# Optimization experiments

Hardware: AMD Instinct MI355X
Metric: run time of the kernel (lower is better)

## Reference

```python
import jax, jax.numpy as jnp
import numpy as np

B, S, H = 4, 2048, 768
NUM_POS = B * (S // 4)  # fixed count of positive clc_label entries (2048, even)
NEG_BIG = -1000000000.0


def setup_inputs() -> dict:
    key = jax.random.key(0)
    k1, k2, k3, k4, k5 = jax.random.split(key, 5)
    encoded_states = jax.random.normal(k1, (B, S, H), dtype=jnp.float32)
    # sorted cell-ids -> contiguous segments for the equality mask
    indicator = jnp.sort(jax.random.randint(k2, (B, S), 0, 256, dtype=jnp.int32), axis=-1)
    # clc_label: first S//4 positions per row are positive targets (class ids in [1,S)),
    # last S//2 positions are -1 (attendable keys), rest 0 (ignored)
    pos_labels = jax.random.randint(k3, (B, S // 4), 1, S, dtype=jnp.int32)
    clc_label = jnp.zeros((B, S), dtype=jnp.int32)
    clc_label = clc_label.at[:, : S // 4].set(pos_labels)
    clc_label = clc_label.at[:, S // 2:].set(-1)
    # uniform_linear params (torch Linear: y = x @ W.T + b)
    W = jax.random.normal(k4, (H, H), dtype=jnp.float32) / np.sqrt(H)
    b = jax.random.normal(k5, (H,), dtype=jnp.float32) * 0.01
    return {"encoded_states": encoded_states, "W": W, "b": b,
            "indicator": indicator, "clc_label": clc_label}


def _ce(logits, labels):
    # mean cross entropy; all labels are > 0 here so ignore_index=0 never triggers
    logp = jax.nn.log_softmax(logits, axis=-1)
    return -jnp.take_along_axis(logp, labels[:, None], axis=1).mean()


def reference(encoded_states, W, b, indicator, clc_label):
    # indicator-equality mask matmul == within-segment sum (the segment-reduce emulation)
    seg_mask = (indicator[:, :, None] == indicator[:, None, :]).astype(encoded_states.dtype)  # [B,S,S]
    agg = jnp.einsum("bij,bjh->bih", seg_mask, encoded_states)  # [B,S,H]
    # Q and K use the SAME linear on the same input -> compute once
    proj = jnp.tanh(agg @ W.T + b)  # [B,S,H]
    scores = jnp.einsum("bih,bjh->bij", proj, proj)  # [B,S,S]
    # attend only to positions where clc_label < 0
    allow = (clc_label < 0)[:, None, :]  # [B,1,S]
    scores = scores + jnp.where(allow, 0.0, NEG_BIG).astype(scores.dtype)
    flat = scores.reshape(-1, S)          # [B*S, S]
    labels = clc_label.reshape(-1)        # [B*S]
    pos_idx = jnp.nonzero(labels > 0, size=NUM_POS)[0]  # row-major order == torch bool-indexing
    logits = flat[pos_idx]                # [NUM_POS, S]
    labs = labels[pos_idx]                # [NUM_POS]
    sep_logits, sep_labels = logits[0::2], labs[0::2]
    tok_logits, tok_labels = logits[1::2], labs[1::2]
    sep_loss = _ce(sep_logits, sep_labels)
    tok_loss = _ce(tok_logits, tok_labels)
    sep_correct = jnp.sum((jnp.argmax(sep_logits, axis=-1).astype(jnp.int32) == sep_labels).astype(jnp.float32))
    tok_correct = jnp.sum((jnp.argmax(tok_logits, axis=-1).astype(jnp.int32) == tok_labels).astype(jnp.float32))
    sep_count = jnp.asarray(sep_logits.shape[0] + 1e-6, dtype=jnp.float32)
    tok_count = jnp.asarray(tok_logits.shape[0] + 1e-6, dtype=jnp.float32)
    return ((sep_loss, sep_correct, sep_count), (tok_loss, tok_correct, tok_count))
```

## Files before the change

### kernel.cpp

```cpp
#include <hip/hip_runtime.h>
#include <math.h>
#include <limits.h>

#define BB 4
#define SS 2048
#define HH 768
#define MAXSEG 256
#define NUM_POS (BB*(SS/4))
#define NEG_BIG -1000000000.0f

typedef _Float16 f16x8 __attribute__((ext_vector_type(8)));
typedef _Float16 f16x4 __attribute__((ext_vector_type(4)));
typedef float    f32x4 __attribute__((ext_vector_type(4)));

__global__ __launch_bounds__(256) void k_scan(
    const int* __restrict__ ind, const int* __restrict__ clc,
    int* __restrict__ seg_id, int* __restrict__ seg_start,
    int* __restrict__ nseg, int* __restrict__ pos_local, int* __restrict__ pos_cnt,
    int* __restrict__ allowCnt, int* __restrict__ firstAllow)
{
  int b = blockIdx.x, t = threadIdx.x;
  int lane = t & 63, wid = t >> 6;
  __shared__ int sInd[SS];
  __shared__ int sWave[4];
  __shared__ int sAC[MAXSEG];
  __shared__ int sFA[MAXSEG];
  for (int i = t; i < SS; i += 256) sInd[i] = ind[b*SS + i];
  sAC[t] = 0; sFA[t] = INT_MAX;
  __syncthreads();

  int i0 = t * 8;
  int f[8], cv[8];
  int lsum = 0;
  #pragma unroll
  for (int u = 0; u < 8; u++) {
    int i = i0 + u;
    f[u] = (i == 0) ? 0 : (sInd[i] != sInd[i-1]);
    cv[u] = clc[b*SS + i];
    lsum += f[u];
  }
  int x = lsum;
  #pragma unroll
  for (int off = 1; off < 64; off <<= 1) {
    int v = __shfl_up(x, off, 64);
    if (lane >= off) x += v;
  }
  if (lane == 63) sWave[wid] = x;
  __syncthreads();
  int base = 0;
  for (int w = 0; w < wid; w++) base += sWave[w];
  int run = base + x - lsum;
  int rid[8];
  #pragma unroll
  for (int u = 0; u < 8; u++) {
    int i = i0 + u;
    run += f[u];
    rid[u] = run;
    seg_id[b*SS + i] = run;
    if (f[u] || i == 0) seg_start[b*(MAXSEG+1) + run] = i;
  }
  if (t == 255) { nseg[b] = run + 1; seg_start[b*(MAXSEG+1) + run + 1] = SS; }

  #pragma unroll
  for (int u = 0; u < 8; u++) {
    if (cv[u] < 0) {
      atomicAdd(&sAC[rid[u]], 1);
      atomicMin(&sFA[rid[u]], i0 + u);
    }
  }
  __syncthreads();
  allowCnt[b*MAXSEG + t]   = sAC[t];
  firstAllow[b*MAXSEG + t] = sFA[t];

  int psum = 0;
  int p[8];
  #pragma unroll
  for (int u = 0; u < 8; u++) { p[u] = (cv[u] > 0) ? 1 : 0; psum += p[u]; }
  x = psum;
  #pragma unroll
  for (int off = 1; off < 64; off <<= 1) {
    int v = __shfl_up(x, off, 64);
    if (lane >= off) x += v;
  }
  __syncthreads();
  if (lane == 63) sWave[wid] = x;
  __syncthreads();
  base = 0;
  for (int w = 0; w < wid; w++) base += sWave[w];
  int rank = base + x - psum;
  #pragma unroll
  for (int u = 0; u < 8; u++) {
    if (p[u]) { pos_local[b*SS + rank] = i0 + u; rank++; }
  }
  if (t == 255) pos_cnt[b] = rank;
}

__global__ __launch_bounds__(256) void k_segsum(
    const float* __restrict__ es, const float* __restrict__ W,
    const int* __restrict__ seg_start, const int* __restrict__ nseg,
    _Float16* __restrict__ segsum_h, _Float16* __restrict__ Wh)
{
  int blk = blockIdx.x, t = threadIdx.x;
  if (blk >= BB*MAXSEG) {
    int idx = (blk - BB*MAXSEG)*256 + t;
    float4 v = ((const float4*)W)[idx];
    f16x4 h;
    h[0] = (_Float16)v.x; h[1] = (_Float16)v.y;
    h[2] = (_Float16)v.z; h[3] = (_Float16)v.w;
    *(f16x4*)(Wh + (size_t)idx*4) = h;
    return;
  }
  int b = blk >> 8, s = blk & 255;
  _Float16* o = segsum_h + ((size_t)b*MAXSEG + s)*HH;
  if (s >= nseg[b]) {
    o[t] = (_Float16)0.f; o[t+256] = (_Float16)0.f; o[t+512] = (_Float16)0.f;
    return;
  }
  int st = seg_start[b*(MAXSEG+1) + s];
  int en = seg_start[b*(MAXSEG+1) + s + 1];
  const float* base = es + (size_t)b*SS*HH;
  float a0 = 0.f, a1 = 0.f, a2 = 0.f;
  for (int i = st; i < en; i++) {
    const float* r = base + (size_t)i*HH;
    a0 += r[t]; a1 += r[t+256]; a2 += r[t+512];
  }
  o[t] = (_Float16)a0; o[t+256] = (_Float16)a1; o[t+512] = (_Float16)a2;
}

__global__ __launch_bounds__(256) void k_gemmU(
    const _Float16* __restrict__ Ah, const _Float16* __restrict__ Wh,
    const float* __restrict__ bias, _Float16* __restrict__ Uh)
{
  int tid = threadIdx.x;
  int w = tid >> 6, lane = tid & 63;
  int tile = blockIdx.x*4 + w;
  int tm = tile / 24, tn = tile % 24;
  int rb = tm*32, cb = tn*32;
  int m0 = lane & 15, quad = lane >> 4;
  const _Float16* A0 = Ah + (size_t)(rb + m0)*HH + quad*8;
  const _Float16* A1 = A0 + (size_t)16*HH;
  const _Float16* B0 = Wh + (size_t)(cb + m0)*HH + quad*8;
  const _Float16* B1 = B0 + (size_t)16*HH;
  f32x4 acc00 = {0.f,0.f,0.f,0.f}, acc01 = {0.f,0.f,0.f,0.f};
  f32x4 acc10 = {0.f,0.f,0.f,0.f}, acc11 = {0.f,0.f,0.f,0.f};
  #pragma unroll 4
  for (int k0 = 0; k0 < HH; k0 += 32) {
    f16x8 a0 = *(const f16x8*)(A0 + k0);
    f16x8 a1 = *(const f16x8*)(A1 + k0);
    f16x8 b0 = *(const f16x8*)(B0 + k0);
    f16x8 b1 = *(const f16x8*)(B1 + k0);
    acc00 = __builtin_amdgcn_mfma_f32_16x16x32_f16(a0, b0, acc00, 0, 0, 0);
    acc01 = __builtin_amdgcn_mfma_f32_16x16x32_f16(a0, b1, acc01, 0, 0, 0);
    acc10 = __builtin_amdgcn_mfma_f32_16x16x32_f16(a1, b0, acc10, 0, 0, 0);
    acc11 = __builtin_amdgcn_mfma_f32_16x16x32_f16(a1, b1, acc11, 0, 0, 0);
  }
  float bc0 = bias[cb + m0], bc1 = bias[cb + 16 + m0];
  int r0 = rb + quad*4;
  #pragma unroll
  for (int i = 0; i < 4; i++) {
    Uh[(size_t)(r0+i)*HH    + cb + m0]      = (_Float16)tanhf(acc00[i] + bc0);
    Uh[(size_t)(r0+i)*HH    + cb + 16 + m0] = (_Float16)tanhf(acc01[i] + bc1);
    Uh[(size_t)(r0+16+i)*HH + cb + m0]      = (_Float16)tanhf(acc10[i] + bc0);
    Uh[(size_t)(r0+16+i)*HH + cb + 16 + m0] = (_Float16)tanhf(acc11[i] + bc1);
  }
}

__global__ __launch_bounds__(256) void k_gram(
    const _Float16* __restrict__ Uh, float* __restrict__ G)
{
  int tid = threadIdx.x;
  int w = tid >> 6, lane = tid & 63;
  int tile = blockIdx.x*4 + w;
  int b = tile >> 8, rem = tile & 255;
  int rb = (rem >> 4)*16, cb = (rem & 15)*16;
  int m0 = lane & 15, quad = lane >> 4;
  const _Float16* Ub = Uh + (size_t)b*MAXSEG*HH;
  const _Float16* A0 = Ub + (size_t)(rb + m0)*HH + quad*8;
  const _Float16* B0 = Ub + (size_t)(cb + m0)*HH + quad*8;
  f32x4 acc = {0.f,0.f,0.f,0.f};
  #pragma unroll 4
  for (int k0 = 0; k0 < HH; k0 += 32) {
    f16x8 a  = *(const f16x8*)(A0 + k0);
    f16x8 bb = *(const f16x8*)(B0 + k0);
    acc = __builtin_amdgcn_mfma_f32_16x16x32_f16(a, bb, acc, 0, 0, 0);
  }
  float* Gb = G + (size_t)b*MAXSEG*MAXSEG;
  int r0 = rb + quad*4;
  #pragma unroll
  for (int i = 0; i < 4; i++)
    Gb[(size_t)(r0+i)*MAXSEG + cb + m0] = acc[i];
}

__global__ __launch_bounds__(256) void k_seglse(
    const float* __restrict__ G, const int* __restrict__ allowCnt,
    const int* __restrict__ firstAllow, const int* __restrict__ nseg,
    float* __restrict__ lse, int* __restrict__ amax)
{
  int lane = threadIdx.x & 63, wid = threadIdx.x >> 6;
  int row = blockIdx.x * 4 + wid;
  int b = row >> 8, si = row & 255;
  if (si >= nseg[b]) return;
  const float* g = G + ((size_t)b*MAXSEG + si)*MAXSEG;
  const int* ac = allowCnt + b*MAXSEG;
  const int* fa = firstAllow + b*MAXSEG;

  float gv[4]; int av[4], fv[4];
  #pragma unroll
  for (int q = 0; q < 4; q++) {
    int s = lane + 64*q;
    gv[q] = g[s]; av[q] = ac[s]; fv[q] = fa[s];
  }
  float m = -INFINITY;
  #pragma unroll
  for (int q = 0; q < 4; q++) if (av[q] > 0) m = fmaxf(m, gv[q]);
  #pragma unroll
  for (int off = 32; off > 0; off >>= 1) m = fmaxf(m, __shfl_xor(m, off, 64));
  float s = 0.f;
  #pragma unroll
  for (int q = 0; q < 4; q++) if (av[q] > 0) s += (float)av[q] * expf(gv[q] - m);
  #pragma unroll
  for (int off = 32; off > 0; off >>= 1) s += __shfl_xor(s, off, 64);
  float bv = -INFINITY; int bi = INT_MAX;
  #pragma unroll
  for (int q = 0; q < 4; q++) {
    if (av[q] > 0 && (gv[q] > bv || (gv[q] == bv && fv[q] < bi))) { bv = gv[q]; bi = fv[q]; }
  }
  #pragma unroll
  for (int off = 32; off > 0; off >>= 1) {
    float ov = __shfl_xor(bv, off, 64);
    int   oi = __shfl_xor(bi, off, 64);
    if (ov > bv || (ov == bv && oi < bi)) { bv = ov; bi = oi; }
  }
  if (lane == 0) {
    lse[row]  = m + logf(s);
    amax[row] = bi;
  }
}

__global__ __launch_bounds__(256) void k_posfinal(
    const float* __restrict__ G, const int* __restrict__ seg_id,
    const int* __restrict__ clc, const int* __restrict__ pos_local,
    const int* __restrict__ pos_cnt, const float* __restrict__ lse,
    const int* __restrict__ amax, float* __restrict__ out)
{
  __shared__ int sBase[BB+1];
  __shared__ float sL0[4], sC0[4], sL1[4], sC1[4];
  int t = threadIdx.x;
  if (t == 0) {
    int acc = 0; sBase[0] = 0;
    for (int b = 0; b < BB; b++) { acc += pos_cnt[b]; sBase[b+1] = acc; }
  }
  __syncthreads();
  int total = sBase[BB];
  if (total > NUM_POS) total = NUM_POS;
  float l0 = 0.f, c0 = 0.f, l1 = 0.f, c1 = 0.f;
  for (int r = t; r < total; r += 256) {
    int b = 0;
    while (b < BB-1 && r >= sBase[b+1]) b++;
    int k = r - sBase[b];
    int i  = pos_local[b*SS + k];
    int si = seg_id[b*SS + i];
    int L  = clc[b*SS + i];
    int sL = seg_id[b*SS + L];
    float vL = G[((size_t)b*MAXSEG + si)*MAXSEG + sL] + (clc[b*SS + L] < 0 ? 0.0f : NEG_BIG);
    float loss = lse[b*MAXSEG + si] - vL;
    float corr = (amax[b*MAXSEG + si] == L) ? 1.0f : 0.0f;
    if (r & 1) { l1 += loss; c1 += corr; } else { l0 += loss; c0 += corr; }
  }
  int lane = t & 63, wid = t >> 6;
  #pragma unroll
  for (int off = 32; off > 0; off >>= 1) {
    l0 += __shfl_down(l0, off, 64);
    c0 += __shfl_down(c0, off, 64);
    l1 += __shfl_down(l1, off, 64);
    c1 += __shfl_down(c1, off, 64);
  }
  if (lane == 0) { sL0[wid] = l0; sC0[wid] = c0; sL1[wid] = l1; sC1[wid] = c1; }
  __syncthreads();
  if (t == 0) {
    float L0 = sL0[0]+sL0[1]+sL0[2]+sL0[3];
    float C0 = sC0[0]+sC0[1]+sC0[2]+sC0[3];
    float L1 = sL1[0]+sL1[1]+sL1[2]+sL1[3];
    float C1 = sC1[0]+sC1[1]+sC1[2]+sC1[3];
    float n = (float)(NUM_POS/2);
    out[0] = L0 / n;
    out[1] = C0;
    out[2] = n + 1e-6f;
    out[3] = L1 / n;
    out[4] = C1;
    out[5] = n + 1e-6f;
  }
}

extern "C" void kernel_launch(void* const* d_in, const int* in_sizes, int n_in,
                              void* d_out, int out_size, void* d_ws, size_t ws_size,
                              hipStream_t stream)
{
  const float* es   = (const float*)d_in[0];
  const float* W    = (const float*)d_in[1];
  const float* bias = (const float*)d_in[2];
  const int*   ind  = (const int*)d_in[3];
  const int*   clc  = (const int*)d_in[4];
  float* out = (float*)d_out;

  char* ws = (char*)d_ws;
  int*   nseg       = (int*)(ws + 0);
  int*   pos_cnt    = (int*)(ws + 256);
  int*   seg_start  = (int*)(ws + 1024);
  int*   seg_id     = (int*)(ws + 8192);
  int*   pos_local  = (int*)(ws + 40960);
  int*   allowCnt   = (int*)(ws + 73728);
  int*   firstAllow = (int*)(ws + 77824);
  float* lse        = (float*)(ws + 81920);
  int*   amax       = (int*)(ws + 86016);
  _Float16* segsum_h = (_Float16*)(ws + 90112);
  _Float16* Wh       = (_Float16*)(ws + 1662976);
  _Float16* Uh       = (_Float16*)(ws + 2842624);
  float*    G        = (float*)(ws + 4415488);

  k_scan<<<BB, 256, 0, stream>>>(ind, clc, seg_id, seg_start, nseg, pos_local,
                                 pos_cnt, allowCnt, firstAllow);
  k_segsum<<<BB*MAXSEG + 576, 256, 0, stream>>>(es, W, seg_start, nseg, segsum_h, Wh);
  k_gemmU<<<192, 256, 0, stream>>>(segsum_h, Wh, bias, Uh);
  k_gram<<<256, 256, 0, stream>>>(Uh, G);
  k_seglse<<<(BB*MAXSEG)/4, 256, 0, stream>>>(G, allowCnt, firstAllow, nseg, lse, amax);
  k_posfinal<<<1, 256, 0, stream>>>(G, seg_id, clc, pos_local, pos_cnt, lse, amax, out);
}
```

Before: 122.9 us.

## Fuse six kernel stages into one cooperative persistent kernel with grid syncs

```diff
diff --git a/kernel.cpp b/kernel.cpp
--- a/kernel.cpp
+++ b/kernel.cpp
@@ -1,6 +1,9 @@
 #include <hip/hip_runtime.h>
+#include <hip/hip_cooperative_groups.h>
 #include <math.h>
 #include <limits.h>
+
+namespace cg = cooperative_groups;
 
 #define BB 4
 #define SS 2048
@@ -13,297 +16,12 @@
 typedef _Float16 f16x4 __attribute__((ext_vector_type(4)));
 typedef float    f32x4 __attribute__((ext_vector_type(4)));
 
-__global__ __launch_bounds__(256) void k_scan(
-    const int* __restrict__ ind, const int* __restrict__ clc,
-    int* __restrict__ seg_id, int* __restrict__ seg_start,
-    int* __restrict__ nseg, int* __restrict__ pos_local, int* __restrict__ pos_cnt,
-    int* __restrict__ allowCnt, int* __restrict__ firstAllow)
+__global__ __launch_bounds__(256, 2) void k_fused(
+    const float* __restrict__ es, const float* __restrict__ W,
+    const float* __restrict__ bias, const int* __restrict__ ind,
+    const int* __restrict__ clc, float* __restrict__ out,
+    char* __restrict__ ws)
 {
-  int b = blockIdx.x, t = threadIdx.x;
-  int lane = t & 63, wid = t >> 6;
-  __shared__ int sInd[SS];
-  __shared__ int sWave[4];
-  __shared__ int sAC[MAXSEG];
-  __shared__ int sFA[MAXSEG];
-  for (int i = t; i < SS; i += 256) sInd[i] = ind[b*SS + i];
-  sAC[t] = 0; sFA[t] = INT_MAX;
-  __syncthreads();
-
-  int i0 = t * 8;
-  int f[8], cv[8];
-  int lsum = 0;
-  #pragma unroll
-  for (int u = 0; u < 8; u++) {
-    int i = i0 + u;
-    f[u] = (i == 0) ? 0 : (sInd[i] != sInd[i-1]);
-    cv[u] = clc[b*SS + i];
-    lsum += f[u];
-  }
-  int x = lsum;
-  #pragma unroll
-  for (int off = 1; off < 64; off <<= 1) {
-    int v = __shfl_up(x, off, 64);
-    if (lane >= off) x += v;
-  }
-  if (lane == 63) sWave[wid] = x;
-  __syncthreads();
-  int base = 0;
-  for (int w = 0; w < wid; w++) base += sWave[w];
-  int run = base + x - lsum;
-  int rid[8];
-  #pragma unroll
-  for (int u = 0; u < 8; u++) {
-    int i = i0 + u;
-    run += f[u];
-    rid[u] = run;
-    seg_id[b*SS + i] = run;
-    if (f[u] || i == 0) seg_start[b*(MAXSEG+1) + run] = i;
-  }
-  if (t == 255) { nseg[b] = run + 1; seg_start[b*(MAXSEG+1) + run + 1] = SS; }
-
-  #pragma unroll
-  for (int u = 0; u < 8; u++) {
-    if (cv[u] < 0) {
-      atomicAdd(&sAC[rid[u]], 1);
-      atomicMin(&sFA[rid[u]], i0 + u);
-    }
-  }
-  __syncthreads();
-  allowCnt[b*MAXSEG + t]   = sAC[t];
-  firstAllow[b*MAXSEG + t] = sFA[t];
-
-  int psum = 0;
-  int p[8];
-  #pragma unroll
-  for (int u = 0; u < 8; u++) { p[u] = (cv[u] > 0) ? 1 : 0; psum += p[u]; }
-  x = psum;
-  #pragma unroll
-  for (int off = 1; off < 64; off <<= 1) {
-    int v = __shfl_up(x, off, 64);
-    if (lane >= off) x += v;
-  }
-  __syncthreads();
-  if (lane == 63) sWave[wid] = x;
-  __syncthreads();
-  base = 0;
-  for (int w = 0; w < wid; w++) base += sWave[w];
-  int rank = base + x - psum;
-  #pragma unroll
-  for (int u = 0; u < 8; u++) {
-    if (p[u]) { pos_local[b*SS + rank] = i0 + u; rank++; }
-  }
-  if (t == 255) pos_cnt[b] = rank;
-}
-
-__global__ __launch_bounds__(256) void k_segsum(
-    const float* __restrict__ es, const float* __restrict__ W,
-    const int* __restrict__ seg_start, const int* __restrict__ nseg,
-    _Float16* __restrict__ segsum_h, _Float16* __restrict__ Wh)
-{
-  int blk = blockIdx.x, t = threadIdx.x;
-  if (blk >= BB*MAXSEG) {
-    int idx = (blk - BB*MAXSEG)*256 + t;
-    float4 v = ((const float4*)W)[idx];
-    f16x4 h;
-    h[0] = (_Float16)v.x; h[1] = (_Float16)v.y;
-    h[2] = (_Float16)v.z; h[3] = (_Float16)v.w;
-    *(f16x4*)(Wh + (size_t)idx*4) = h;
-    return;
-  }
-  int b = blk >> 8, s = blk & 255;
-  _Float16* o = segsum_h + ((size_t)b*MAXSEG + s)*HH;
-  if (s >= nseg[b]) {
-    o[t] = (_Float16)0.f; o[t+256] = (_Float16)0.f; o[t+512] = (_Float16)0.f;
-    return;
-  }
-  int st = seg_start[b*(MAXSEG+1) + s];
-  int en = seg_start[b*(MAXSEG+1) + s + 1];
-  const float* base = es + (size_t)b*SS*HH;
-  float a0 = 0.f, a1 = 0.f, a2 = 0.f;
-  for (int i = st; i < en; i++) {
-    const float* r = base + (size_t)i*HH;
-    a0 += r[t]; a1 += r[t+256]; a2 += r[t+512];
-  }
-  o[t] = (_Float16)a0; o[t+256] = (_Float16)a1; o[t+512] = (_Float16)a2;
-}
-
-__global__ __launch_bounds__(256) void k_gemmU(
-    const _Float16* __restrict__ Ah, const _Float16* __restrict__ Wh,
-    const float* __restrict__ bias, _Float16* __restrict__ Uh)
-{
-  int tid = threadIdx.x;
-  int w = tid >> 6, lane = tid & 63;
-  int tile = blockIdx.x*4 + w;
-  int tm = tile / 24, tn = tile % 24;
-  int rb = tm*32, cb = tn*32;
-  int m0 = lane & 15, quad = lane >> 4;
-  const _Float16* A0 = Ah + (size_t)(rb + m0)*HH + quad*8;
-  const _Float16* A1 = A0 + (size_t)16*HH;
-  const _Float16* B0 = Wh + (size_t)(cb + m0)*HH + quad*8;
-  const _Float16* B1 = B0 + (size_t)16*HH;
-  f32x4 acc00 = {0.f,0.f,0.f,0.f}, acc01 = {0.f,0.f,0.f,0.f};
-  f32x4 acc10 = {0.f,0.f,0.f,0.f}, acc11 = {0.f,0.f,0.f,0.f};
-  #pragma unroll 4
-  for (int k0 = 0; k0 < HH; k0 += 32) {
-    f16x8 a0 = *(const f16x8*)(A0 + k0);
-    f16x8 a1 = *(const f16x8*)(A1 + k0);
-    f16x8 b0 = *(const f16x8*)(B0 + k0);
-    f16x8 b1 = *(const f16x8*)(B1 + k0);
-    acc00 = __builtin_amdgcn_mfma_f32_16x16x32_f16(a0, b0, acc00, 0, 0, 0);
-    acc01 = __builtin_amdgcn_mfma_f32_16x16x32_f16(a0, b1, acc01, 0, 0, 0);
-    acc10 = __builtin_amdgcn_mfma_f32_16x16x32_f16(a1, b0, acc10, 0, 0, 0);
-    acc11 = __builtin_amdgcn_mfma_f32_16x16x32_f16(a1, b1, acc11, 0, 0, 0);
-  }
-  float bc0 = bias[cb + m0], bc1 = bias[cb + 16 + m0];
-  int r0 = rb + quad*4;
-  #pragma unroll
-  for (int i = 0; i < 4; i++) {
-    Uh[(size_t)(r0+i)*HH    + cb + m0]      = (_Float16)tanhf(acc00[i] + bc0);
-    Uh[(size_t)(r0+i)*HH    + cb + 16 + m0] = (_Float16)tanhf(acc01[i] + bc1);
-    Uh[(size_t)(r0+16+i)*HH + cb + m0]      = (_Float16)tanhf(acc10[i] + bc0);
-    Uh[(size_t)(r0+16+i)*HH + cb + 16 + m0] = (_Float16)tanhf(acc11[i] + bc1);
-  }
-}
-
-__global__ __launch_bounds__(256) void k_gram(
-    const _Float16* __restrict__ Uh, float* __restrict__ G)
-{
-  int tid = threadIdx.x;
-  int w = tid >> 6, lane = tid & 63;
-  int tile = blockIdx.x*4 + w;
-  int b = tile >> 8, rem = tile & 255;
-  int rb = (rem >> 4)*16, cb = (rem & 15)*16;
-  int m0 = lane & 15, quad = lane >> 4;
-  const _Float16* Ub = Uh + (size_t)b*MAXSEG*HH;
-  const _Float16* A0 = Ub + (size_t)(rb + m0)*HH + quad*8;
-  const _Float16* B0 = Ub + (size_t)(cb + m0)*HH + quad*8;
-  f32x4 acc = {0.f,0.f,0.f,0.f};
-  #pragma unroll 4
-  for (int k0 = 0; k0 < HH; k0 += 32) {
-    f16x8 a  = *(const f16x8*)(A0 + k0);
-    f16x8 bb = *(const f16x8*)(B0 + k0);
-    acc = __builtin_amdgcn_mfma_f32_16x16x32_f16(a, bb, acc, 0, 0, 0);
-  }
-  float* Gb = G + (size_t)b*MAXSEG*MAXSEG;
-  int r0 = rb + quad*4;
-  #pragma unroll
-  for (int i = 0; i < 4; i++)
-    Gb[(size_t)(r0+i)*MAXSEG + cb + m0] = acc[i];
-}
-
-__global__ __launch_bounds__(256) void k_seglse(
-    const float* __restrict__ G, const int* __restrict__ allowCnt,
-    const int* __restrict__ firstAllow, const int* __restrict__ nseg,
-    float* __restrict__ lse, int* __restrict__ amax)
-{
-  int lane = threadIdx.x & 63, wid = threadIdx.x >> 6;
-  int row = blockIdx.x * 4 + wid;
-  int b = row >> 8, si = row & 255;
-  if (si >= nseg[b]) return;
-  const float* g = G + ((size_t)b*MAXSEG + si)*MAXSEG;
-  const int* ac = allowCnt + b*MAXSEG;
-  const int* fa = firstAllow + b*MAXSEG;
-
-  float gv[4]; int av[4], fv[4];
-  #pragma unroll
-  for (int q = 0; q < 4; q++) {
-    int s = lane + 64*q;
-    gv[q] = g[s]; av[q] = ac[s]; fv[q] = fa[s];
-  }
-  float m = -INFINITY;
-  #pragma unroll
-  for (int q = 0; q < 4; q++) if (av[q] > 0) m = fmaxf(m, gv[q]);
-  #pragma unroll
-  for (int off = 32; off > 0; off >>= 1) m = fmaxf(m, __shfl_xor(m, off, 64));
-  float s = 0.f;
-  #pragma unroll
-  for (int q = 0; q < 4; q++) if (av[q] > 0) s += (float)av[q] * expf(gv[q] - m);
-  #pragma unroll
-  for (int off = 32; off > 0; off >>= 1) s += __shfl_xor(s, off, 64);
-  float bv = -INFINITY; int bi = INT_MAX;
-  #pragma unroll
-  for (int q = 0; q < 4; q++) {
-    if (av[q] > 0 && (gv[q] > bv || (gv[q] == bv && fv[q] < bi))) { bv = gv[q]; bi = fv[q]; }
-  }
-  #pragma unroll
-  for (int off = 32; off > 0; off >>= 1) {
-    float ov = __shfl_xor(bv, off, 64);
-    int   oi = __shfl_xor(bi, off, 64);
-    if (ov > bv || (ov == bv && oi < bi)) { bv = ov; bi = oi; }
-  }
-  if (lane == 0) {
-    lse[row]  = m + logf(s);
-    amax[row] = bi;
-  }
-}
-
-__global__ __launch_bounds__(256) void k_posfinal(
-    const float* __restrict__ G, const int* __restrict__ seg_id,
-    const int* __restrict__ clc, const int* __restrict__ pos_local,
-    const int* __restrict__ pos_cnt, const float* __restrict__ lse,
-    const int* __restrict__ amax, float* __restrict__ out)
-{
-  __shared__ int sBase[BB+1];
-  __shared__ float sL0[4], sC0[4], sL1[4], sC1[4];
-  int t = threadIdx.x;
-  if (t == 0) {
-    int acc = 0; sBase[0] = 0;
-    for (int b = 0; b < BB; b++) { acc += pos_cnt[b]; sBase[b+1] = acc; }
-  }
-  __syncthreads();
-  int total = sBase[BB];
-  if (total > NUM_POS) total = NUM_POS;
-  float l0 = 0.f, c0 = 0.f, l1 = 0.f, c1 = 0.f;
-  for (int r = t; r < total; r += 256) {
-    int b = 0;
-    while (b < BB-1 && r >= sBase[b+1]) b++;
-    int k = r - sBase[b];
-    int i  = pos_local[b*SS + k];
-    int si = seg_id[b*SS + i];
-    int L  = clc[b*SS + i];
-    int sL = seg_id[b*SS + L];
-    float vL = G[((size_t)b*MAXSEG + si)*MAXSEG + sL] + (clc[b*SS + L] < 0 ? 0.0f : NEG_BIG);
-    float loss = lse[b*MAXSEG + si] - vL;
-    float corr = (amax[b*MAXSEG + si] == L) ? 1.0f : 0.0f;
-    if (r & 1) { l1 += loss; c1 += corr; } else { l0 += loss; c0 += corr; }
-  }
-  int lane = t & 63, wid = t >> 6;
-  #pragma unroll
-  for (int off = 32; off > 0; off >>= 1) {
-    l0 += __shfl_down(l0, off, 64);
-    c0 += __shfl_down(c0, off, 64);
-    l1 += __shfl_down(l1, off, 64);
-    c1 += __shfl_down(c1, off, 64);
-  }
-  if (lane == 0) { sL0[wid] = l0; sC0[wid] = c0; sL1[wid] = l1; sC1[wid] = c1; }
-  __syncthreads();
-  if (t == 0) {
-    float L0 = sL0[0]+sL0[1]+sL0[2]+sL0[3];
-    float C0 = sC0[0]+sC0[1]+sC0[2]+sC0[3];
-    float L1 = sL1[0]+sL1[1]+sL1[2]+sL1[3];
-    float C1 = sC1[0]+sC1[1]+sC1[2]+sC1[3];
-    float n = (float)(NUM_POS/2);
-    out[0] = L0 / n;
-    out[1] = C0;
-    out[2] = n + 1e-6f;
-    out[3] = L1 / n;
-    out[4] = C1;
-    out[5] = n + 1e-6f;
-  }
-}
-
-extern "C" void kernel_launch(void* const* d_in, const int* in_sizes, int n_in,
-                              void* d_out, int out_size, void* d_ws, size_t ws_size,
-                              hipStream_t stream)
-{
-  const float* es   = (const float*)d_in[0];
-  const float* W    = (const float*)d_in[1];
-  const float* bias = (const float*)d_in[2];
-  const int*   ind  = (const int*)d_in[3];
-  const int*   clc  = (const int*)d_in[4];
-  float* out = (float*)d_out;
-
-  char* ws = (char*)d_ws;
   int*   nseg       = (int*)(ws + 0);
   int*   pos_cnt    = (int*)(ws + 256);
   int*   seg_start  = (int*)(ws + 1024);
@@ -318,11 +36,294 @@
   _Float16* Uh       = (_Float16*)(ws + 2842624);
   float*    G        = (float*)(ws + 4415488);
 
-  k_scan<<<BB, 256, 0, stream>>>(ind, clc, seg_id, seg_start, nseg, pos_local,
-                                 pos_cnt, allowCnt, firstAllow);
-  k_segsum<<<BB*MAXSEG + 576, 256, 0, stream>>>(es, W, seg_start, nseg, segsum_h, Wh);
-  k_gemmU<<<192, 256, 0, stream>>>(segsum_h, Wh, bias, Uh);
-  k_gram<<<256, 256, 0, stream>>>(Uh, G);
-  k_seglse<<<(BB*MAXSEG)/4, 256, 0, stream>>>(G, allowCnt, firstAllow, nseg, lse, amax);
-  k_posfinal<<<1, 256, 0, stream>>>(G, seg_id, clc, pos_local, pos_cnt, lse, amax, out);
+  cg::grid_group grid = cg::this_grid();
+  const int t = threadIdx.x;
+  const int lane = t & 63, wid = t >> 6;
+  const int nblk = (int)gridDim.x;
+
+  __shared__ int sInd[SS];
+  __shared__ int sWave[4];
+  __shared__ int sAC[MAXSEG];
+  __shared__ int sFA[MAXSEG];
+  __shared__ int sBase[BB+1];
+  __shared__ float sL0[4], sC0[4], sL1[4], sC1[4];
+
+  if (blockIdx.x < BB) {
+    int b = blockIdx.x;
+    for (int i = t; i < SS; i += 256) sInd[i] = ind[b*SS + i];
+    sAC[t] = 0; sFA[t] = INT_MAX;
+    __syncthreads();
+
+    int i0 = t * 8;
+    int f[8], cv[8];
+    int lsum = 0;
+    #pragma unroll
+    for (int u = 0; u < 8; u++) {
+      int i = i0 + u;
+      f[u] = (i == 0) ? 0 : (sInd[i] != sInd[i-1]);
+      cv[u] = clc[b*SS + i];
+      lsum += f[u];
+    }
+    int x = lsum;
+    #pragma unroll
+    for (int off = 1; off < 64; off <<= 1) {
+      int v = __shfl_up(x, off, 64);
+      if (lane >= off) x += v;
+    }
+    if (lane == 63) sWave[wid] = x;
+    __syncthreads();
+    int base = 0;
+    for (int w = 0; w < wid; w++) base += sWave[w];
+    int run = base + x - lsum;
+    int rid[8];
+    #pragma unroll
+    for (int u = 0; u < 8; u++) {
+      int i = i0 + u;
+      run += f[u];
+      rid[u] = run;
+      seg_id[b*SS + i] = run;
+      if (f[u] || i == 0) seg_start[b*(MAXSEG+1) + run] = i;
+    }
+    if (t == 255) { nseg[b] = run + 1; seg_start[b*(MAXSEG+1) + run + 1] = SS; }
+
+    #pragma unroll
+    for (int u = 0; u < 8; u++) {
+      if (cv[u] < 0) {
+        atomicAdd(&sAC[rid[u]], 1);
+        atomicMin(&sFA[rid[u]], i0 + u);
+      }
+    }
+    __syncthreads();
+    allowCnt[b*MAXSEG + t]   = sAC[t];
+    firstAllow[b*MAXSEG + t] = sFA[t];
+
+    int psum = 0;
+    int p[8];
+    #pragma unroll
+    for (int u = 0; u < 8; u++) { p[u] = (cv[u] > 0) ? 1 : 0; psum += p[u]; }
+    x = psum;
+    #pragma unroll
+    for (int off = 1; off < 64; off <<= 1) {
+      int v = __shfl_up(x, off, 64);
+      if (lane >= off) x += v;
+    }
+    __syncthreads();
+    if (lane == 63) sWave[wid] = x;
+    __syncthreads();
+    base = 0;
+    for (int w = 0; w < wid; w++) base += sWave[w];
+    int rank = base + x - psum;
+    #pragma unroll
+    for (int u = 0; u < 8; u++) {
+      if (p[u]) { pos_local[b*SS + rank] = i0 + u; rank++; }
+    }
+    if (t == 255) pos_cnt[b] = rank;
+  }
+  grid.sync();
+
+  for (int blk = blockIdx.x; blk < BB*MAXSEG + 576; blk += nblk) {
+    if (blk >= BB*MAXSEG) {
+      int idx = (blk - BB*MAXSEG)*256 + t;
+      float4 v = ((const float4*)W)[idx];
+      f16x4 h;
+      h[0] = (_Float16)v.x; h[1] = (_Float16)v.y;
+      h[2] = (_Float16)v.z; h[3] = (_Float16)v.w;
+      *(f16x4*)(Wh + (size_t)idx*4) = h;
+    } else {
+      int b = blk >> 8, s = blk & 255;
+      _Float16* o = segsum_h + ((size_t)b*MAXSEG + s)*HH;
+      if (s >= nseg[b]) {
+        o[t] = (_Float16)0.f; o[t+256] = (_Float16)0.f; o[t+512] = (_Float16)0.f;
+      } else {
+        int st = seg_start[b*(MAXSEG+1) + s];
+        int en = seg_start[b*(MAXSEG+1) + s + 1];
+        const float* bp = es + (size_t)b*SS*HH;
+        float a0 = 0.f, a1 = 0.f, a2 = 0.f;
+        for (int i = st; i < en; i++) {
+          const float* r = bp + (size_t)i*HH;
+          a0 += r[t]; a1 += r[t+256]; a2 += r[t+512];
+        }
+        o[t] = (_Float16)a0; o[t+256] = (_Float16)a1; o[t+512] = (_Float16)a2;
+      }
+    }
+  }
+  grid.sync();
+
+  {
+    int gw = blockIdx.x*4 + wid;
+    for (int tile = gw; tile < 768; tile += nblk*4) {
+      int tm = tile / 24, tn = tile % 24;
+      int rb = tm*32, cb = tn*32;
+      int m0 = lane & 15, quad = lane >> 4;
+      const _Float16* A0 = segsum_h + (size_t)(rb + m0)*HH + quad*8;
+      const _Float16* A1 = A0 + (size_t)16*HH;
+      const _Float16* B0 = Wh + (size_t)(cb + m0)*HH + quad*8;
+      const _Float16* B1 = B0 + (size_t)16*HH;
+      f32x4 acc00 = {0.f,0.f,0.f,0.f}, acc01 = {0.f,0.f,0.f,0.f};
+      f32x4 acc10 = {0.f,0.f,0.f,0.f}, acc11 = {0.f,0.f,0.f,0.f};
+      #pragma unroll 4
+      for (int k0 = 0; k0 < HH; k0 += 32) {
+        f16x8 a0 = *(const f16x8*)(A0 + k0);
+        f16x8 a1 = *(const f16x8*)(A1 + k0);
+        f16x8 b0 = *(const f16x8*)(B0 + k0);
+        f16x8 b1 = *(const f16x8*)(B1 + k0);
+        acc00 = __builtin_amdgcn_mfma_f32_16x16x32_f16(a0, b0, acc00, 0, 0, 0);
+        acc01 = __builtin_amdgcn_mfma_f32_16x16x32_f16(a0, b1, acc01, 0, 0, 0);
+        acc10 = __builtin_amdgcn_mfma_f32_16x16x32_f16(a1, b0, acc10, 0, 0, 0);
+        acc11 = __builtin_amdgcn_mfma_f32_16x16x32_f16(a1, b1, acc11, 0, 0, 0);
+      }
+      float bc0 = bias[cb + m0], bc1 = bias[cb + 16 + m0];
+      int r0 = rb + quad*4;
+      #pragma unroll
+      for (int i = 0; i < 4; i++) {
+        Uh[(size_t)(r0+i)*HH    + cb + m0]      = (_Float16)tanhf(acc00[i] + bc0);
+        Uh[(size_t)(r0+i)*HH    + cb + 16 + m0] = (_Float16)tanhf(acc01[i] + bc1);
+        Uh[(size_t)(r0+16+i)*HH + cb + m0]      = (_Float16)tanhf(acc10[i] + bc0);
+        Uh[(size_t)(r0+16+i)*HH + cb + 16 + m0] = (_Float16)tanhf(acc11[i] + bc1);
+      }
+    }
+  }
+  grid.sync();
+
+  {
+    int gw = blockIdx.x*4 + wid;
+    for (int tile = gw; tile < BB*256; tile += nblk*4) {
+      int b = tile >> 8, rem = tile & 255;
+      int rb = (rem >> 4)*16, cb = (rem & 15)*16;
+      int m0 = lane & 15, quad = lane >> 4;
+      const _Float16* Ub = Uh + (size_t)b*MAXSEG*HH;
+      const _Float16* A0 = Ub + (size_t)(rb + m0)*HH + quad*8;
+      const _Float16* B0 = Ub + (size_t)(cb + m0)*HH + quad*8;
+      f32x4 acc = {0.f,0.f,0.f,0.f};
+      #pragma unroll 4
+      for (int k0 = 0; k0 < HH; k0 += 32) {
+        f16x8 a  = *(const f16x8*)(A0 + k0);
+        f16x8 bb = *(const f16x8*)(B0 + k0);
+        acc = __builtin_amdgcn_mfma_f32_16x16x32_f16(a, bb, acc, 0, 0, 0);
+      }
+      float* Gb = G + (size_t)b*MAXSEG*MAXSEG;
+      int r0 = rb + quad*4;
+      #pragma unroll
+      for (int i = 0; i < 4; i++)
+        Gb[(size_t)(r0+i)*MAXSEG + cb + m0] = acc[i];
+    }
+  }
+  grid.sync();
+
+  {
+    int gw = blockIdx.x*4 + wid;
+    for (int row = gw; row < BB*MAXSEG; row += nblk*4) {
+      int b = row >> 8, si = row & 255;
+      if (si < nseg[b]) {
+        const float* g = G + ((size_t)b*MAXSEG + si)*MAXSEG;
+        const int* ac = allowCnt + b*MAXSEG;
+        const int* fa = firstAllow + b*MAXSEG;
+        float gv[4]; int av[4], fv[4];
+        #pragma unroll
+        for (int q = 0; q < 4; q++) {
+          int s = lane + 64*q;
+          gv[q] = g[s]; av[q] = ac[s]; fv[q] = fa[s];
+        }
+        float m = -INFINITY;
+        #pragma unroll
+        for (int q = 0; q < 4; q++) if (av[q] > 0) m = fmaxf(m, gv[q]);
+        #pragma unroll
+        for (int off = 32; off > 0; off >>= 1) m = fmaxf(m, __shfl_xor(m, off, 64));
+        float s = 0.f;
+        #pragma unroll
+        for (int q = 0; q < 4; q++) if (av[q] > 0) s += (float)av[q] * expf(gv[q] - m);
+        #pragma unroll
+        for (int off = 32; off > 0; off >>= 1) s += __shfl_xor(s, off, 64);
+        float bv = -INFINITY; int bi = INT_MAX;
+        #pragma unroll
+        for (int q = 0; q < 4; q++) {
+          if (av[q] > 0 && (gv[q] > bv || (gv[q] == bv && fv[q] < bi))) { bv = gv[q]; bi = fv[q]; }
+        }
+        #pragma unroll
+        for (int off = 32; off > 0; off >>= 1) {
+          float ov = __shfl_xor(bv, off, 64);
+          int   oi = __shfl_xor(bi, off, 64);
+          if (ov > bv || (ov == bv && oi < bi)) { bv = ov; bi = oi; }
+        }
+        if (lane == 0) {
+          lse[row]  = m + logf(s);
+          amax[row] = bi;
+        }
+      }
+    }
+  }
+  grid.sync();
+
+  if (blockIdx.x == 0) {
+    if (t == 0) {
+      int acc = 0; sBase[0] = 0;
+      for (int b = 0; b < BB; b++) { acc += pos_cnt[b]; sBase[b+1] = acc; }
+    }
+    __syncthreads();
+    int total = sBase[BB];
+    if (total > NUM_POS) total = NUM_POS;
+    float l0 = 0.f, c0 = 0.f, l1 = 0.f, c1 = 0.f;
+    for (int r = t; r < total; r += 256) {
+      int b = 0;
+      while (b < BB-1 && r >= sBase[b+1]) b++;
+      int k = r - sBase[b];
+      int i  = pos_local[b*SS + k];
+      int si = seg_id[b*SS + i];
+      int L  = clc[b*SS + i];
+      int sL = seg_id[b*SS + L];
+      float vL = G[((size_t)b*MAXSEG + si)*MAXSEG + sL] + (clc[b*SS + L] < 0 ? 0.0f : NEG_BIG);
+      float loss = lse[b*MAXSEG + si] - vL;
+      float corr = (amax[b*MAXSEG + si] == L) ? 1.0f : 0.0f;
+      if (r & 1) { l1 += loss; c1 += corr; } else { l0 += loss; c0 += corr; }
+    }
+    #pragma unroll
+    for (int off = 32; off > 0; off >>= 1) {
+      l0 += __shfl_down(l0, off, 64);
+      c0 += __shfl_down(c0, off, 64);
+      l1 += __shfl_down(l1, off, 64);
+      c1 += __shfl_down(c1, off, 64);
+    }
+    if (lane == 0) { sL0[wid] = l0; sC0[wid] = c0; sL1[wid] = l1; sC1[wid] = c1; }
+    __syncthreads();
+    if (t == 0) {
+      float L0 = sL0[0]+sL0[1]+sL0[2]+sL0[3];
+      float C0 = sC0[0]+sC0[1]+sC0[2]+sC0[3];
+      float L1 = sL1[0]+sL1[1]+sL1[2]+sL1[3];
+      float C1 = sC1[0]+sC1[1]+sC1[2]+sC1[3];
+      float n = (float)(NUM_POS/2);
+      out[0] = L0 / n;
+      out[1] = C0;
+      out[2] = n + 1e-6f;
+      out[3] = L1 / n;
+      out[4] = C1;
+      out[5] = n + 1e-6f;
+    }
+  }
 }
+
+extern "C" void kernel_launch(void* const* d_in, const int* in_sizes, int n_in,
+                              void* d_out, int out_size, void* d_ws, size_t ws_size,
+                              hipStream_t stream)
+{
+  const float* es   = (const float*)d_in[0];
+  const float* W    = (const float*)d_in[1];
+  const float* bias = (const float*)d_in[2];
+  const int*   ind  = (const int*)d_in[3];
+  const int*   clc  = (const int*)d_in[4];
+  float* out = (float*)d_out;
+  char*  wsp = (char*)d_ws;
+
+  static int grid = 0;
+  if (grid == 0) {
+    int nb = 0;
+    hipOccupancyMaxActiveBlocksPerMultiprocessor(&nb, k_fused, 256, 0);
+    if (nb < 1) nb = 1;
+    grid = nb * 256;
+    if (grid > 512) grid = 512;
+    if (grid < 4) grid = 4;
+  }
+
+  void* args[] = {(void*)&es, (void*)&W, (void*)&bias, (void*)&ind,
+                  (void*)&clc, (void*)&out, (void*)&wsp};
+  hipLaunchCooperativeKernel(k_fused, dim3(grid), dim3(256), args, 0, stream);
+}
```

Measured after the change: 393.1 us. 3.2x slower.

## Fuse gram and segment LSE kernels, move W cast into scan, unroll segsum

Applied to the files above, without the earlier changes.

```diff
diff --git a/kernel.cpp b/kernel.cpp
--- a/kernel.cpp
+++ b/kernel.cpp
@@ -13,13 +13,24 @@
 typedef _Float16 f16x4 __attribute__((ext_vector_type(4)));
 typedef float    f32x4 __attribute__((ext_vector_type(4)));
 
-__global__ __launch_bounds__(256) void k_scan(
+__global__ __launch_bounds__(256) void k_scanW(
     const int* __restrict__ ind, const int* __restrict__ clc,
+    const float* __restrict__ W, _Float16* __restrict__ Wh,
     int* __restrict__ seg_id, int* __restrict__ seg_start,
     int* __restrict__ nseg, int* __restrict__ pos_local, int* __restrict__ pos_cnt,
     int* __restrict__ allowCnt, int* __restrict__ firstAllow)
 {
-  int b = blockIdx.x, t = threadIdx.x;
+  int t = threadIdx.x;
+  if (blockIdx.x >= BB) {
+    int idx = (blockIdx.x - BB)*256 + t;
+    float4 v = ((const float4*)W)[idx];
+    f16x4 h;
+    h[0] = (_Float16)v.x; h[1] = (_Float16)v.y;
+    h[2] = (_Float16)v.z; h[3] = (_Float16)v.w;
+    *(f16x4*)(Wh + (size_t)idx*4) = h;
+    return;
+  }
+  int b = blockIdx.x;
   int lane = t & 63, wid = t >> 6;
   __shared__ int sInd[SS];
   __shared__ int sWave[4];
@@ -96,20 +107,11 @@
 }
 
 __global__ __launch_bounds__(256) void k_segsum(
-    const float* __restrict__ es, const float* __restrict__ W,
+    const float* __restrict__ es,
     const int* __restrict__ seg_start, const int* __restrict__ nseg,
-    _Float16* __restrict__ segsum_h, _Float16* __restrict__ Wh)
+    _Float16* __restrict__ segsum_h)
 {
   int blk = blockIdx.x, t = threadIdx.x;
-  if (blk >= BB*MAXSEG) {
-    int idx = (blk - BB*MAXSEG)*256 + t;
-    float4 v = ((const float4*)W)[idx];
-    f16x4 h;
-    h[0] = (_Float16)v.x; h[1] = (_Float16)v.y;
-    h[2] = (_Float16)v.z; h[3] = (_Float16)v.w;
-    *(f16x4*)(Wh + (size_t)idx*4) = h;
-    return;
-  }
   int b = blk >> 8, s = blk & 255;
   _Float16* o = segsum_h + ((size_t)b*MAXSEG + s)*HH;
   if (s >= nseg[b]) {
@@ -120,11 +122,27 @@
   int en = seg_start[b*(MAXSEG+1) + s + 1];
   const float* base = es + (size_t)b*SS*HH;
   float a0 = 0.f, a1 = 0.f, a2 = 0.f;
-  for (int i = st; i < en; i++) {
+  float b0 = 0.f, b1 = 0.f, b2 = 0.f;
+  float c0 = 0.f, c1 = 0.f, c2 = 0.f;
+  float d0 = 0.f, d1 = 0.f, d2 = 0.f;
+  int i = st;
+  for (; i + 4 <= en; i += 4) {
+    const float* r0 = base + (size_t)i*HH;
+    const float* r1 = r0 + HH;
+    const float* r2 = r1 + HH;
+    const float* r3 = r2 + HH;
+    a0 += r0[t]; a1 += r0[t+256]; a2 += r0[t+512];
+    b0 += r1[t]; b1 += r1[t+256]; b2 += r1[t+512];
+    c0 += r2[t]; c1 += r2[t+256]; c2 += r2[t+512];
+    d0 += r3[t]; d1 += r3[t+256]; d2 += r3[t+512];
+  }
+  for (; i < en; i++) {
     const float* r = base + (size_t)i*HH;
     a0 += r[t]; a1 += r[t+256]; a2 += r[t+512];
   }
-  o[t] = (_Float16)a0; o[t+256] = (_Float16)a1; o[t+512] = (_Float16)a2;
+  o[t]     = (_Float16)((a0 + b0) + (c0 + d0));
+  o[t+256] = (_Float16)((a1 + b1) + (c1 + d1));
+  o[t+512] = (_Float16)((a2 + b2) + (c2 + d2));
 }
 
 __global__ __launch_bounds__(256) void k_gemmU(
@@ -165,75 +183,95 @@
   }
 }
 
-__global__ __launch_bounds__(256) void k_gram(
-    const _Float16* __restrict__ Uh, float* __restrict__ G)
-{
-  int tid = threadIdx.x;
-  int w = tid >> 6, lane = tid & 63;
-  int tile = blockIdx.x*4 + w;
-  int b = tile >> 8, rem = tile & 255;
-  int rb = (rem >> 4)*16, cb = (rem & 15)*16;
+__global__ __launch_bounds__(256) void k_gramlse(
+    const _Float16* __restrict__ Uh, const int* __restrict__ allowCnt,
+    const int* __restrict__ firstAllow, const int* __restrict__ nseg,
+    float* __restrict__ G, float* __restrict__ lse, int* __restrict__ amax)
+{
+  __shared__ float sG[16][257];
+  int t = threadIdx.x;
+  int lane = t & 63, w = t >> 6;
+  int blk = blockIdx.x;
+  int b = blk >> 4;
+  int rb = (blk & 15) * 16;
   int m0 = lane & 15, quad = lane >> 4;
   const _Float16* Ub = Uh + (size_t)b*MAXSEG*HH;
   const _Float16* A0 = Ub + (size_t)(rb + m0)*HH + quad*8;
-  const _Float16* B0 = Ub + (size_t)(cb + m0)*HH + quad*8;
-  f32x4 acc = {0.f,0.f,0.f,0.f};
+  int cb0 = w * 64;
+  const _Float16* B0 = Ub + (size_t)(cb0      + m0)*HH + quad*8;
+  const _Float16* B1 = Ub + (size_t)(cb0 + 16 + m0)*HH + quad*8;
+  const _Float16* B2 = Ub + (size_t)(cb0 + 32 + m0)*HH + quad*8;
+  const _Float16* B3 = Ub + (size_t)(cb0 + 48 + m0)*HH + quad*8;
+  f32x4 acc0 = {0.f,0.f,0.f,0.f}, acc1 = {0.f,0.f,0.f,0.f};
+  f32x4 acc2 = {0.f,0.f,0.f,0.f}, acc3 = {0.f,0.f,0.f,0.f};
   #pragma unroll 4
   for (int k0 = 0; k0 < HH; k0 += 32) {
     f16x8 a  = *(const f16x8*)(A0 + k0);
-    f16x8 bb = *(const f16x8*)(B0 + k0);
-    acc = __builtin_amdgcn_mfma_f32_16x16x32_f16(a, bb, acc, 0, 0, 0);
+    f16x8 q0 = *(const f16x8*)(B0 + k0);
+    f16x8 q1 = *(const f16x8*)(B1 + k0);
+    f16x8 q2 = *(const f16x8*)(B2 + k0);
+    f16x8 q3 = *(const f16x8*)(B3 + k0);
+    acc0 = __builtin_amdgcn_mfma_f32_16x16x32_f16(a, q0, acc0, 0, 0, 0);
+    acc1 = __builtin_amdgcn_mfma_f32_16x16x32_f16(a, q1, acc1, 0, 0, 0);
+    acc2 = __builtin_amdgcn_mfma_f32_16x16x32_f16(a, q2, acc2, 0, 0, 0);
+    acc3 = __builtin_amdgcn_mfma_f32_16x16x32_f16(a, q3, acc3, 0, 0, 0);
   }
   float* Gb = G + (size_t)b*MAXSEG*MAXSEG;
-  int r0 = rb + quad*4;
-  #pragma unroll
-  for (int i = 0; i < 4; i++)
-    Gb[(size_t)(r0+i)*MAXSEG + cb + m0] = acc[i];
-}
-
-__global__ __launch_bounds__(256) void k_seglse(
-    const float* __restrict__ G, const int* __restrict__ allowCnt,
-    const int* __restrict__ firstAllow, const int* __restrict__ nseg,
-    float* __restrict__ lse, int* __restrict__ amax)
-{
-  int lane = threadIdx.x & 63, wid = threadIdx.x >> 6;
-  int row = blockIdx.x * 4 + wid;
-  int b = row >> 8, si = row & 255;
-  if (si >= nseg[b]) return;
-  const float* g = G + ((size_t)b*MAXSEG + si)*MAXSEG;
+  int r0 = quad*4;
+  #pragma unroll
+  for (int i = 0; i < 4; i++) {
+    int rl = r0 + i;
+    sG[rl][cb0      + m0] = acc0[i];
+    sG[rl][cb0 + 16 + m0] = acc1[i];
+    sG[rl][cb0 + 32 + m0] = acc2[i];
+    sG[rl][cb0 + 48 + m0] = acc3[i];
+    float* gr = Gb + (size_t)(rb + rl)*MAXSEG;
+    gr[cb0      + m0] = acc0[i];
+    gr[cb0 + 16 + m0] = acc1[i];
+    gr[cb0 + 32 + m0] = acc2[i];
+    gr[cb0 + 48 + m0] = acc3[i];
+  }
+  __syncthreads();
+
   const int* ac = allowCnt + b*MAXSEG;
   const int* fa = firstAllow + b*MAXSEG;
-
-  float gv[4]; int av[4], fv[4];
-  #pragma unroll
-  for (int q = 0; q < 4; q++) {
-    int s = lane + 64*q;
-    gv[q] = g[s]; av[q] = ac[s]; fv[q] = fa[s];
-  }
-  float m = -INFINITY;
-  #pragma unroll
-  for (int q = 0; q < 4; q++) if (av[q] > 0) m = fmaxf(m, gv[q]);
-  #pragma unroll
-  for (int off = 32; off > 0; off >>= 1) m = fmaxf(m, __shfl_xor(m, off, 64));
-  float s = 0.f;
-  #pragma unroll
-  for (int q = 0; q < 4; q++) if (av[q] > 0) s += (float)av[q] * expf(gv[q] - m);
-  #pragma unroll
-  for (int off = 32; off > 0; off >>= 1) s += __shfl_xor(s, off, 64);
-  float bv = -INFINITY; int bi = INT_MAX;
-  #pragma unroll
-  for (int q = 0; q < 4; q++) {
-    if (av[q] > 0 && (gv[q] > bv || (gv[q] == bv && fv[q] < bi))) { bv = gv[q]; bi = fv[q]; }
-  }
-  #pragma unroll
-  for (int off = 32; off > 0; off >>= 1) {
-    float ov = __shfl_xor(bv, off, 64);
-    int   oi = __shfl_xor(bi, off, 64);
-    if (ov > bv || (ov == bv && oi < bi)) { bv = ov; bi = oi; }
-  }
-  if (lane == 0) {
-    lse[row]  = m + logf(s);
-    amax[row] = bi;
+  int ns = nseg[b];
+  #pragma unroll
+  for (int j = 0; j < 4; j++) {
+    int rl = w*4 + j;
+    int si = rb + rl;
+    if (si >= ns) continue;
+    float gv[4]; int av[4], fv[4];
+    #pragma unroll
+    for (int q = 0; q < 4; q++) {
+      int s = lane + 64*q;
+      gv[q] = sG[rl][s]; av[q] = ac[s]; fv[q] = fa[s];
+    }
+    float m = -INFINITY;
+    #pragma unroll
+    for (int q = 0; q < 4; q++) if (av[q] > 0) m = fmaxf(m, gv[q]);
+    #pragma unroll
+    for (int off = 32; off > 0; off >>= 1) m = fmaxf(m, __shfl_xor(m, off, 64));
+    float s = 0.f;
+    #pragma unroll
+    for (int q = 0; q < 4; q++) if (av[q] > 0) s += (float)av[q] * expf(gv[q] - m);
+    #pragma unroll
+    for (int off = 32; off > 0; off >>= 1) s += __shfl_xor(s, off, 64);
+    float bv = -INFINITY; int bi = INT_MAX;
+    #pragma unroll
+    for (int q = 0; q < 4; q++) {
+      if (av[q] > 0 && (gv[q] > bv || (gv[q] == bv && fv[q] < bi))) { bv = gv[q]; bi = fv[q]; }
+    }
+    #pragma unroll
+    for (int off = 32; off > 0; off >>= 1) {
+      float ov = __shfl_xor(bv, off, 64);
+      int   oi = __shfl_xor(bi, off, 64);
+      if (ov > bv || (ov == bv && oi < bi)) { bv = ov; bi = oi; }
+    }
+    if (lane == 0) {
+      lse[b*MAXSEG + si]  = m + logf(s);
+      amax[b*MAXSEG + si] = bi;
+    }
   }
 }
 
@@ -318,11 +356,10 @@
   _Float16* Uh       = (_Float16*)(ws + 2842624);
   float*    G        = (float*)(ws + 4415488);
 
-  k_scan<<<BB, 256, 0, stream>>>(ind, clc, seg_id, seg_start, nseg, pos_local,
-                                 pos_cnt, allowCnt, firstAllow);
-  k_segsum<<<BB*MAXSEG + 576, 256, 0, stream>>>(es, W, seg_start, nseg, segsum_h, Wh);
+  k_scanW<<<BB + 576, 256, 0, stream>>>(ind, clc, W, Wh, seg_id, seg_start,
+                                        nseg, pos_local, pos_cnt, allowCnt, firstAllow);
+  k_segsum<<<BB*MAXSEG, 256, 0, stream>>>(es, seg_start, nseg, segsum_h);
   k_gemmU<<<192, 256, 0, stream>>>(segsum_h, Wh, bias, Uh);
-  k_gram<<<256, 256, 0, stream>>>(Uh, G);
-  k_seglse<<<(BB*MAXSEG)/4, 256, 0, stream>>>(G, allowCnt, firstAllow, nseg, lse, amax);
+  k_gramlse<<<BB*16, 256, 0, stream>>>(Uh, allowCnt, firstAllow, nseg, G, lse, amax);
   k_posfinal<<<1, 256, 0, stream>>>(G, seg_id, clc, pos_local, pos_cnt, lse, amax, out);
 }
```

Result: slower. 133.8 us (+8.9%).
